# Optimization experiments

Measured on AMD Instinct MI355X. Metric: run time of the kernel, lower is better.

The kernel has to match this reference:

```python
import jax, jax.numpy as jnp
import numpy as np

N = 100000   # nodes
E = 3200000  # edges
G = 1024     # graphs in the batch
H = 64       # hidden_dim


def setup_inputs() -> dict:
    key = jax.random.key(0)
    ks = jax.random.split(key, 12)
    x = jax.random.normal(ks[0], (N, 1), dtype=jnp.float32)
    edge_index = jax.random.randint(ks[1], (2, E), 0, N, dtype=jnp.int32)
    batch = jnp.sort(jax.random.randint(ks[2], (N,), 0, G, dtype=jnp.int32))
    s = 0.1
    w1 = jax.random.normal(ks[3], (1, H), dtype=jnp.float32) * s
    b1 = jnp.zeros((H,), dtype=jnp.float32)
    w2 = jax.random.normal(ks[4], (H, H), dtype=jnp.float32) * s
    b2 = jnp.zeros((H,), dtype=jnp.float32)
    w3 = jax.random.normal(ks[5], (H, H), dtype=jnp.float32) * s
    b3 = jnp.zeros((H,), dtype=jnp.float32)
    fc_w = jax.random.normal(ks[6], (H, 1), dtype=jnp.float32) * s
    fc_b = jnp.zeros((1,), dtype=jnp.float32)
    return {"x": x, "edge_index": edge_index, "batch": batch,
            "w1": w1, "b1": b1, "w2": w2, "b2": b2, "w3": w3, "b3": b3,
            "fc_w": fc_w, "fc_b": fc_b}


def _gcn_norm(edge_index, n):
    # add self-loops: A_hat = A + I
    src = jnp.concatenate([edge_index[0], jnp.arange(n, dtype=edge_index.dtype)])
    dst = jnp.concatenate([edge_index[1], jnp.arange(n, dtype=edge_index.dtype)])
    deg = jax.ops.segment_sum(jnp.ones_like(dst, dtype=jnp.float32), dst, num_segments=n)
    dinv = jnp.where(deg > 0, jax.lax.rsqrt(deg), 0.0)
    norm = dinv[src] * dinv[dst]  # [E+N]
    return src, dst, norm


def _gcn_conv(x, w, b, src, dst, norm, n):
    h = x @ w                               # [N, H] transform first (PyG order)
    msg = h[src] * norm[:, None]            # gather + scale  [E+N, H]
    out = jax.ops.segment_sum(msg, dst, num_segments=n)  # scatter-add
    return out + b


def reference(x, edge_index, batch, w1, b1, w2, b2, w3, b3, fc_w, fc_b):
    n = x.shape[0]
    src, dst, norm = _gcn_norm(edge_index, n)
    h = jax.nn.relu(_gcn_conv(x, w1, b1, src, dst, norm, n))
    h = jax.nn.relu(_gcn_conv(h, w2, b2, src, dst, norm, n))
    h = jax.nn.relu(_gcn_conv(h, w3, b3, src, dst, norm, n))
    # global mean pool over graphs
    sums = jax.ops.segment_sum(h, batch, num_segments=G)                 # [G, H]
    cnts = jax.ops.segment_sum(jnp.ones((n,), jnp.float32), batch, num_segments=G)
    pooled = sums / jnp.maximum(cnts, 1.0)[:, None]
    return pooled @ fc_w + fc_b  # [G, 1]
```

## Files before the change

kernel.cpp:

```cpp
#include <hip/hip_runtime.h>
#include <hip/hip_bf16.h>


#define WS_ALIGN(x) (((x) + 255) & ~size_t(255))
#define NCHUNK 8
#define CSH 14
#define NB 32
#define RPW (NB / 4)
#define USH 17
#define UMASK 0x1FFFF
#define BKTMAX 256
#define SBS 512
#define SBKEYS (SBS * NCHUNK)
#define P1T 2048
#define PADGAP 1540

__device__ __forceinline__ float bf2f(unsigned short h) {
    union { unsigned u; float f; } t;
    t.u = ((unsigned)h) << 16;
    return t.f;
}
__device__ __forceinline__ unsigned short f2bf(float f) {
    union { float f; unsigned u; } t;
    t.f = f;
    unsigned r = t.u + 0x7FFF + ((t.u >> 16) & 1);
    return (unsigned short)(r >> 16);
}
__device__ __forceinline__ float bfLo(unsigned v) {
    union { unsigned u; float f; } t;
    t.u = v << 16;
    return t.f;
}
__device__ __forceinline__ float bfHi(unsigned v) {
    union { unsigned u; float f; } t;
    t.u = v & 0xFFFF0000u;
    return t.f;
}

__global__ __launch_bounds__(256) void k_zero(int g, int n, int* bucketCnt,
                                              int* gCursor, float* xs,
                                              unsigned short* bufA,
                                              unsigned short* bufB,
                                              float* gsum, float* gcnt) {
    int i = blockIdx.x * blockDim.x + threadIdx.x;
    if (i < BKTMAX) { bucketCnt[i] = 0; gCursor[i] = 0; }
    if (i < g) { gsum[i] = 0.f; gcnt[i] = 0.f; }
    if (i < 64) {
        bufA[(size_t)n * 64 + i] = 0;
        bufB[(size_t)n * 64 + i] = 0;
    }
    if (i == 0) xs[n] = 0.f;
}

__global__ __launch_bounds__(256) void k_cnt1(int e, const int* __restrict__ dst,
                                              int* __restrict__ bucketCnt) {
    __shared__ int c[BKTMAX];
    int tid = threadIdx.x;
    c[tid] = 0;
    __syncthreads();
    int base = blockIdx.x * P1T;
#pragma unroll
    for (int q = 0; q < P1T / 256; ++q) {
        int i = base + q * 256 + tid;
        if (i < e) atomicAdd(&c[dst[i] >> 9], 1);
    }
    __syncthreads();
    if (c[tid] > 0) atomicAdd(&bucketCnt[tid], c[tid]);
}

__global__ __launch_bounds__(256) void k_scanB(int nbkt, int e,
                                               const int* __restrict__ bucketCnt,
                                               int* __restrict__ bucketStart) {
    __shared__ int sd[256];
    int tid = threadIdx.x;
    int v = (tid < nbkt) ? bucketCnt[tid] : 0;
    sd[tid] = v;
    __syncthreads();
    for (int off = 1; off < 256; off <<= 1) {
        int t = (tid >= off) ? sd[tid - off] : 0;
        __syncthreads();
        sd[tid] += t;
        __syncthreads();
    }
    if (tid < nbkt) bucketStart[tid] = sd[tid] - v;
    if (tid == 0) bucketStart[nbkt] = e;
}

__global__ __launch_bounds__(256) void k_p1(int e, const int* __restrict__ src,
                                            const int* __restrict__ dst,
                                            const int* __restrict__ bucketStart,
                                            int* __restrict__ gCursor,
                                            int* __restrict__ pkbuf) {
    __shared__ int cnt[BKTMAX], exc[BKTMAX], cur[BKTMAX], bb[BKTMAX];
    __shared__ int sd[256];
    __shared__ int stage[P1T];
    __shared__ unsigned char stgb[P1T];
    int tid = threadIdx.x;
    cnt[tid] = 0;
    __syncthreads();
    int base = blockIdx.x * P1T;
    int m = e - base; if (m > P1T) m = P1T;
    int pk8[P1T / 256];
    int b8[P1T / 256];
#pragma unroll
    for (int q = 0; q < P1T / 256; ++q) {
        int li = q * 256 + tid;
        if (li < m) {
            int d = dst[base + li];
            int s = src[base + li];
            int b = d >> 9;
            b8[q] = b;
            pk8[q] = ((d & (SBS - 1)) << USH) | s;
            atomicAdd(&cnt[b], 1);
        }
    }
    __syncthreads();
    int cv = cnt[tid];
    sd[tid] = cv;
    __syncthreads();
    for (int off = 1; off < 256; off <<= 1) {
        int t = (tid >= off) ? sd[tid - off] : 0;
        __syncthreads();
        sd[tid] += t;
        __syncthreads();
    }
    exc[tid] = sd[tid] - cv;
    cur[tid] = sd[tid] - cv;
    if (cv > 0) bb[tid] = atomicAdd(&gCursor[tid], cv);
    __syncthreads();
#pragma unroll
    for (int q = 0; q < P1T / 256; ++q) {
        int li = q * 256 + tid;
        if (li < m) {
            int b = b8[q];
            int pos = atomicAdd(&cur[b], 1);
            stage[pos] = pk8[q];
            stgb[pos] = (unsigned char)b;
        }
    }
    __syncthreads();
#pragma unroll
    for (int q = 0; q < P1T / 256; ++q) {
        int p = q * 256 + tid;
        if (p < m) {
            int b = stgb[p];
            pkbuf[bucketStart[b] + bb[b] + (p - exc[b])] = stage[p];
        }
    }
}

__global__ __launch_bounds__(256) void k_p2(int n, const int* __restrict__ bucketStart,
                                            const int* __restrict__ pkbuf,
                                            const float* __restrict__ x,
                                            int* __restrict__ csr,
                                            int* __restrict__ bndRow,
                                            float* __restrict__ dinv,
                                            float* __restrict__ xs) {
    __shared__ int cnt[SBKEYS + 1];
    __shared__ int sd[256];
    __shared__ int padOff[SBS];
    __shared__ int padTotal_s;
    int sb = blockIdx.x, tid = threadIdx.x;
    int r0 = bucketStart[sb], r1 = bucketStart[sb + 1];
    int r0pad = r0 + sb * PADGAP;
    for (int k = tid; k < SBKEYS + 1; k += 256) cnt[k] = 0;
    __syncthreads();
    for (int i = r0 + tid; i < r1; i += 256) {
        int w = pkbuf[i];
        int key = ((w >> USH) << 3) | ((w & UMASK) >> CSH);
        atomicAdd(&cnt[key], 1);
    }
    __syncthreads();
    int base16 = tid * 16;
    int loc[16]; int s = 0;
#pragma unroll
    for (int j = 0; j < 16; ++j) { loc[j] = cnt[base16 + j]; s += loc[j]; }
    sd[tid] = s;
    __syncthreads();
    for (int off = 1; off < 256; off <<= 1) {
        int t = (tid >= off) ? sd[tid - off] : 0;
        __syncthreads();
        sd[tid] += t;
        __syncthreads();
    }
    int run = sd[tid] - s;
#pragma unroll
    for (int j = 0; j < 16; ++j) { cnt[base16 + j] = run; run += loc[j]; }
    if (tid == 255) cnt[SBKEYS] = run;
    __syncthreads();
    int d0 = tid * 2, d1 = tid * 2 + 1;
    int len0 = cnt[d0 * 8 + 8] - cnt[d0 * 8];
    int len1 = cnt[d1 * 8 + 8] - cnt[d1 * 8];
    int p0 = (-len0) & 3, p1 = (-len1) & 3;
    int tsum = p0 + p1;
    sd[tid] = tsum;
    __syncthreads();
    for (int off = 1; off < 256; off <<= 1) {
        int t = (tid >= off) ? sd[tid - off] : 0;
        __syncthreads();
        sd[tid] += t;
        __syncthreads();
    }
    int pexcl = sd[tid] - tsum;
    padOff[d0] = pexcl;
    padOff[d1] = pexcl + p0;
    if (tid == 255) padTotal_s = pexcl + tsum;
    __syncthreads();
    for (int dl = tid; dl < SBS; dl += 256) {
        int gbi = sb * 16 + (dl >> 5);
        int vi = dl & 31;
        int startp = r0pad + cnt[dl * 8] + padOff[dl];
        bndRow[gbi * 33 + vi] = startp;
        if (vi == 0 && dl > 0) bndRow[(gbi - 1) * 33 + 32] = startp;
        int v = sb * SBS + dl;
        if (v < n) {
            int len = cnt[dl * 8 + 8] - cnt[dl * 8];
            float di = 1.0f / sqrtf((float)(len + 1));
            dinv[v] = di;
            xs[v] = x[v] * di;
        }
        int padc = (-(cnt[dl * 8 + 8] - cnt[dl * 8])) & 3;
        int ps = r0pad + cnt[dl * 8 + 8] + padOff[dl];
        for (int j = 0; j < padc; ++j) csr[ps + j] = n;
    }
    if (tid == 0) {
        int endp = r0pad + cnt[SBKEYS] + padTotal_s;
        bndRow[(sb * 16 + 15) * 33 + 32] = endp;
        csr[endp] = n; csr[endp + 1] = n; csr[endp + 2] = n; csr[endp + 3] = n;
    }
    __syncthreads();
    for (int i = r0 + tid; i < r1; i += 256) {
        int w = pkbuf[i];
        int srcv = w & UMASK;
        int dl = w >> USH;
        int key = (dl << 3) | (srcv >> CSH);
        int pos = atomicAdd(&cnt[key], 1);
        csr[r0pad + pos + padOff[dl]] = srcv;
    }
}

__global__ __launch_bounds__(256, 8) void k_layer1(int n, const int* __restrict__ bndRow,
                                                   const int* __restrict__ csr,
                                                   const float* __restrict__ xs,
                                                   const float* __restrict__ dinv,
                                                   const float* __restrict__ w1,
                                                   const float* __restrict__ b1,
                                                   unsigned short* __restrict__ hs_out) {
    int tid = threadIdx.x;
    int r = tid >> 6, lane = tid & 63;
    float w1r = w1[lane], b1r = b1[lane];
    int wid = blockIdx.x * 4 + r;
    int stride = gridDim.x * 4;
    for (int v = wid; v < n; v += stride) {
        int bi = v >> 5, vi = v & 31;
        int s0 = bndRow[bi * 33 + vi], s1 = bndRow[bi * 33 + vi + 1];
        float acc = 0.f;
        for (int k = s0 + lane; k < s1; k += 64) acc += xs[csr[k]];
#pragma unroll
        for (int m = 32; m > 0; m >>= 1) acc += __shfl_xor(acc, m, 64);
        float dv = dinv[v];
        float s = (acc + xs[v]) * dv;
        hs_out[(size_t)v * 64 + lane] = f2bf(fmaxf(s * w1r + b1r, 0.f) * dv);
    }
}

#define GATHER_CORE                                                            \
    __shared__ float ws[64 * 64];                                              \
    __shared__ float rowl[4][64];                                              \
    __shared__ int bndL[NB + 1];                                               \
    int tid = threadIdx.x;                                                     \
    int lane = tid & 63;                                                       \
    int r = tid >> 6;                                                          \
    int h = lane >> 5;                                                         \
    int fi = lane & 31;                                                        \
    int v0 = blockIdx.x * NB;                                                  \
    const unsigned* hsu = (const unsigned*)hs_in;                              \
    for (int k = tid; k < 64 * 64; k += 256) ws[k] = w[k];                     \
    if (tid < NB + 1) bndL[tid] = bndRow[blockIdx.x * 33 + tid];               \
    float accLo[RPW], accHi[RPW];                                              \
    _Pragma("unroll")                                                          \
    for (int q = 0; q < RPW; ++q) {                                            \
        int v = v0 + q * 4 + r;                                                \
        unsigned sv = (v < n && h == 0) ? hsu[(size_t)v * 32 + fi] : 0u;       \
        accLo[q] = bfLo(sv);                                                   \
        accHi[q] = bfHi(sv);                                                   \
    }                                                                          \
    __syncthreads();                                                           \
    _Pragma("unroll")                                                          \
    for (int t = 0; t < RPW / 2; ++t) {                                        \
        int viA = (2 * t) * 4 + r;                                             \
        int viB = (2 * t + 1) * 4 + r;                                         \
        int ba = __builtin_amdgcn_readfirstlane(bndL[viA]);                    \
        int a1 = __builtin_amdgcn_readfirstlane(bndL[viA + 1]);                \
        int bb = __builtin_amdgcn_readfirstlane(bndL[viB]);                    \
        int b1_ = __builtin_amdgcn_readfirstlane(bndL[viB + 1]);               \
        int pa = (ba < a1) ? ba : bb;                                          \
        int pb = (bb < b1_) ? bb : ba;                                         \
        int uA0 = csr[pa], uA1 = csr[pa + 1], uA2 = csr[pa + 2], uA3 = csr[pa + 3]; \
        int uB0 = csr[pb], uB1 = csr[pb + 1], uB2 = csr[pb + 2], uB3 = csr[pb + 3]; \
        unsigned gA01 = hsu[(size_t)(h ? uA1 : uA0) * 32 + fi];                \
        unsigned gA23 = hsu[(size_t)(h ? uA3 : uA2) * 32 + fi];                \
        unsigned gB01 = hsu[(size_t)(h ? uB1 : uB0) * 32 + fi];                \
        unsigned gB23 = hsu[(size_t)(h ? uB3 : uB2) * 32 + fi];                \
        while (ba < a1 || bb < b1_) {                                          \
            int na = ba + 4, nb = bb + 4;                                      \
            int pa2 = (na < a1) ? na : ((nb < b1_) ? nb : pa);                 \
            int pb2 = (nb < b1_) ? nb : ((na < a1) ? na : pb);                 \
            int vA0 = csr[pa2], vA1 = csr[pa2 + 1], vA2 = csr[pa2 + 2], vA3 = csr[pa2 + 3]; \
            int vB0 = csr[pb2], vB1 = csr[pb2 + 1], vB2 = csr[pb2 + 2], vB3 = csr[pb2 + 3]; \
            unsigned nA01 = hsu[(size_t)(h ? vA1 : vA0) * 32 + fi];            \
            unsigned nA23 = hsu[(size_t)(h ? vA3 : vA2) * 32 + fi];            \
            unsigned nB01 = hsu[(size_t)(h ? vB1 : vB0) * 32 + fi];            \
            unsigned nB23 = hsu[(size_t)(h ? vB3 : vB2) * 32 + fi];            \
                            \
            float mA = (ba < a1) ? 1.f : 0.f;                                  \
            float mB = (bb < b1_) ? 1.f : 0.f;                                 \
            accLo[2 * t]     += (bfLo(gA01) + bfLo(gA23)) * mA;                \
            accHi[2 * t]     += (bfHi(gA01) + bfHi(gA23)) * mA;                \
            accLo[2 * t + 1] += (bfLo(gB01) + bfLo(gB23)) * mB;                \
            accHi[2 * t + 1] += (bfHi(gB01) + bfHi(gB23)) * mB;                \
            gA01 = nA01; gA23 = nA23; gB01 = nB01; gB23 = nB23;                \
            pa = pa2; pb = pb2;                                                \
            ba = na; bb = nb;                                                  \
        }                                                                      \
    }

__global__ __launch_bounds__(256, 4) void k_gg_mid(int n,
                                                   const int* __restrict__ bndRow,
                                                   const int* __restrict__ csr,
                                                   const unsigned short* __restrict__ hs_in,
                                                   const float* __restrict__ dinv,
                                                   const float* __restrict__ w,
                                                   const float* __restrict__ b,
                                                   unsigned short* __restrict__ hs_out) {
    GATHER_CORE
    float breg = b[lane];
#pragma unroll 1
    for (int q = 0; q < RPW; ++q) {
        int v = v0 + q * 4 + r;
        if (v >= n) continue;
        float dv = dinv[v];
        float lo = accLo[q]; lo += __shfl_xor(lo, 32, 64);
        float hi = accHi[q]; hi += __shfl_xor(hi, 32, 64);
        if (h == 0) {
            rowl[r][2 * fi] = lo * dv;
            rowl[r][2 * fi + 1] = hi * dv;
        }
        float o = breg;
#pragma unroll
        for (int k = 0; k < 64; ++k) o += rowl[r][k] * ws[k * 64 + lane];
        hs_out[(size_t)v * 64 + lane] = f2bf(fmaxf(o, 0.f) * dv);
    }
}

__global__ __launch_bounds__(256, 4) void k_gg_final(int n,
                                                     const int* __restrict__ bndRow,
                                                     const int* __restrict__ csr,
                                                     const unsigned short* __restrict__ hs_in,
                                                     const float* __restrict__ dinv,
                                                     const float* __restrict__ w,
                                                     const float* __restrict__ b,
                                                     const float* __restrict__ fcw,
                                                     float* __restrict__ dots) {
    GATHER_CORE
    float breg = b[lane];
    float freg = fcw[lane];
#pragma unroll 1
    for (int q = 0; q < RPW; ++q) {
        int v = v0 + q * 4 + r;
        if (v >= n) continue;
        float dv = dinv[v];
        float lo = accLo[q]; lo += __shfl_xor(lo, 32, 64);
        float hi = accHi[q]; hi += __shfl_xor(hi, 32, 64);
        if (h == 0) {
            rowl[r][2 * fi] = lo * dv;
            rowl[r][2 * fi + 1] = hi * dv;
        }
        float o = breg;
#pragma unroll
        for (int k = 0; k < 64; ++k) o += rowl[r][k] * ws[k * 64 + lane];
        float val = fmaxf(o, 0.f) * freg;
#pragma unroll
        for (int m = 32; m > 0; m >>= 1) val += __shfl_xor(val, m, 64);
        if (lane == 0) dots[v] = val;
    }
}

__global__ __launch_bounds__(256) void k_pool(int n, const float* __restrict__ dots,
                                              const int* __restrict__ batch,
                                              float* __restrict__ gsum,
                                              float* __restrict__ gcnt) {
    __shared__ float ls[64], lc[64];
    __shared__ int gmin_s;
    int tid = threadIdx.x;
    int i0 = blockIdx.x * 1024;
    if (tid == 0) gmin_s = batch[i0];
    if (tid < 64) { ls[tid] = 0.f; lc[tid] = 0.f; }
    __syncthreads();
    int gmin = gmin_s;
#pragma unroll
    for (int c = 0; c < 4; ++c) {
        int i = i0 + c * 256 + tid;
        if (i < n) {
            int g = batch[i];
            float d = dots[i];
            int rr = g - gmin;
            if (rr < 64) {
                atomicAdd(&ls[rr], d);
                atomicAdd(&lc[rr], 1.f);
            } else {
                atomicAdd(&gsum[g], d);
                atomicAdd(&gcnt[g], 1.f);
            }
        }
    }
    __syncthreads();
    if (tid < 64 && lc[tid] != 0.f) {
        atomicAdd(&gsum[gmin + tid], ls[tid]);
        atomicAdd(&gcnt[gmin + tid], lc[tid]);
    }
}

__global__ __launch_bounds__(256) void k_out(int g, const float* __restrict__ gsum,
                                             const float* __restrict__ gcnt,
                                             const float* __restrict__ fcb,
                                             float* __restrict__ out) {
    int i = blockIdx.x * blockDim.x + threadIdx.x;
    if (i < g) out[i] = gsum[i] / fmaxf(gcnt[i], 1.f) + fcb[0];
}

extern "C" void kernel_launch(void* const* d_in, const int* in_sizes, int n_in,
                              void* d_out, int out_size, void* d_ws, size_t ws_size,
                              hipStream_t stream) {
    const float* x    = (const float*)d_in[0];
    const int*   ei   = (const int*)d_in[1];
    const int*   batch= (const int*)d_in[2];
    const float* w1   = (const float*)d_in[3];
    const float* b1   = (const float*)d_in[4];
    const float* w2   = (const float*)d_in[5];
    const float* b2   = (const float*)d_in[6];
    const float* w3   = (const float*)d_in[7];
    const float* b3   = (const float*)d_in[8];
    const float* fcw  = (const float*)d_in[9];
    const float* fcb  = (const float*)d_in[10];
    float* out = (float*)d_out;

    const int N = in_sizes[0];
    const int E = in_sizes[1] / 2;
    const int G = out_size;
    const int H = 64;
    const int nbkt = (N + SBS - 1) / SBS;
    const int NBLK = (N + NB - 1) / NB;
    const int NBLKP = nbkt * 16;

    const int* src = ei;
    const int* dst = ei + E;

    char* p = (char*)d_ws;
    int*   bucketCnt   = (int*)p; p += WS_ALIGN(sizeof(int) * BKTMAX);
    int*   bucketStart = (int*)p; p += WS_ALIGN(sizeof(int) * (BKTMAX + 1));
    int*   gCursor     = (int*)p; p += WS_ALIGN(sizeof(int) * BKTMAX);
    int*   pkbuf       = (int*)p; p += WS_ALIGN(sizeof(int) * (size_t)E);
    int*   csr         = (int*)p; p += WS_ALIGN(sizeof(int) * ((size_t)E + (size_t)nbkt * PADGAP + 8));
    int*   bndRow      = (int*)p; p += WS_ALIGN(sizeof(int) * (size_t)NBLKP * 33);
    float* dinv        = (float*)p; p += WS_ALIGN(sizeof(float) * N);
    float* xs          = (float*)p; p += WS_ALIGN(sizeof(float) * (N + 1));
    unsigned short* bufA = (unsigned short*)p; p += WS_ALIGN(sizeof(unsigned short) * (size_t)(N + 1) * H);
    unsigned short* bufB = (unsigned short*)p; p += WS_ALIGN(sizeof(unsigned short) * (size_t)(N + 1) * H);
    float* dots        = (float*)p; p += WS_ALIGN(sizeof(float) * N);
    float* gsum        = (float*)p; p += WS_ALIGN(sizeof(float) * G);
    float* gcnt        = (float*)p; p += WS_ALIGN(sizeof(float) * G);

    const int B = 256;
    int gridZ    = ((G > BKTMAX ? G : BKTMAX) + B - 1) / B;
    int gridT    = (E + P1T - 1) / P1T;
    int gridG    = (G + B - 1) / B;
    int gridPool = (N + 1023) / 1024;
    int gridPers = 2048;
    if (gridPers * 4 > N) gridPers = (N + 3) / 4;

    k_zero<<<gridZ, B, 0, stream>>>(G, N, bucketCnt, gCursor, xs, bufA, bufB, gsum, gcnt);
    k_cnt1<<<gridT, B, 0, stream>>>(E, dst, bucketCnt);
    k_scanB<<<1, B, 0, stream>>>(nbkt, E, bucketCnt, bucketStart);
    k_p1<<<gridT, B, 0, stream>>>(E, src, dst, bucketStart, gCursor, pkbuf);
    k_p2<<<nbkt, B, 0, stream>>>(N, bucketStart, pkbuf, x, csr, bndRow, dinv, xs);
    k_layer1<<<gridPers, B, 0, stream>>>(N, bndRow, csr, xs, dinv, w1, b1, bufA);
    k_gg_mid<<<NBLK, B, 0, stream>>>(N, bndRow, csr, bufA, dinv, w2, b2, bufB);
    k_gg_final<<<NBLK, B, 0, stream>>>(N, bndRow, csr, bufB, dinv, w3, b3, fcw, dots);
    k_pool<<<gridPool, B, 0, stream>>>(N, dots, batch, gsum, gcnt);
    k_out<<<gridG, B, 0, stream>>>(G, gsum, gcnt, fcb, out);
}
```

Before: 327.2 us.

## Pre-scale CSR indices, pad rows to 8, and use single-row gather loop

Halves the super-bucket size (256 nodes, 512 buckets) so each thread owns one destination row in the CSR build. Rows are now padded to multiples of 8 instead of 4, and source indices are stored pre-shifted by 5 so the gather kernels index the bf16 feature array without a multiply. The gather core now processes one row at a time with an 8-edge software-pipelined loop and skips empty rows, replacing the paired-row loop with masking. The change trades more padding edges and less interleaving of independent rows for simpler addressing and wider per-iteration loads.

```diff
diff --git a/kernel.cpp b/kernel.cpp
--- a/kernel.cpp
+++ b/kernel.cpp
@@ -3,23 +3,17 @@
 
 
 #define WS_ALIGN(x) (((x) + 255) & ~size_t(255))
-#define NCHUNK 8
-#define CSH 14
 #define NB 32
 #define RPW (NB / 4)
 #define USH 17
-#define UMASK 0x1FFFF
-#define BKTMAX 256
-#define SBS 512
+#define BKTMAX 512
+#define SBS 256
+#define NCHUNK 8
+#define CSH 14
 #define SBKEYS (SBS * NCHUNK)
 #define P1T 2048
-#define PADGAP 1540
-
-__device__ __forceinline__ float bf2f(unsigned short h) {
-    union { unsigned u; float f; } t;
-    t.u = ((unsigned)h) << 16;
-    return t.f;
-}
+#define PADGAP 1792
+
 __device__ __forceinline__ unsigned short f2bf(float f) {
     union { float f; unsigned u; } t;
     t.f = f;
@@ -56,16 +50,17 @@
                                               int* __restrict__ bucketCnt) {
     __shared__ int c[BKTMAX];
     int tid = threadIdx.x;
-    c[tid] = 0;
+    c[tid] = 0; c[tid + 256] = 0;
     __syncthreads();
     int base = blockIdx.x * P1T;
 #pragma unroll
     for (int q = 0; q < P1T / 256; ++q) {
         int i = base + q * 256 + tid;
-        if (i < e) atomicAdd(&c[dst[i] >> 9], 1);
+        if (i < e) atomicAdd(&c[dst[i] >> 8], 1);
     }
     __syncthreads();
     if (c[tid] > 0) atomicAdd(&bucketCnt[tid], c[tid]);
+    if (c[tid + 256] > 0) atomicAdd(&bucketCnt[tid + 256], c[tid + 256]);
 }
 
 __global__ __launch_bounds__(256) void k_scanB(int nbkt, int e,
@@ -73,8 +68,11 @@
                                                int* __restrict__ bucketStart) {
     __shared__ int sd[256];
     int tid = threadIdx.x;
-    int v = (tid < nbkt) ? bucketCnt[tid] : 0;
-    sd[tid] = v;
+    int i0 = tid * 2;
+    int v0 = (i0 < nbkt) ? bucketCnt[i0] : 0;
+    int v1 = (i0 + 1 < nbkt) ? bucketCnt[i0 + 1] : 0;
+    int ts = v0 + v1;
+    sd[tid] = ts;
     __syncthreads();
     for (int off = 1; off < 256; off <<= 1) {
         int t = (tid >= off) ? sd[tid - off] : 0;
@@ -82,7 +80,9 @@
         sd[tid] += t;
         __syncthreads();
     }
-    if (tid < nbkt) bucketStart[tid] = sd[tid] - v;
+    int excl = sd[tid] - ts;
+    if (i0 < nbkt) bucketStart[i0] = excl;
+    if (i0 + 1 < nbkt) bucketStart[i0 + 1] = excl + v0;
     if (tid == 0) bucketStart[nbkt] = e;
 }
 
@@ -94,9 +94,9 @@
     __shared__ int cnt[BKTMAX], exc[BKTMAX], cur[BKTMAX], bb[BKTMAX];
     __shared__ int sd[256];
     __shared__ int stage[P1T];
-    __shared__ unsigned char stgb[P1T];
+    __shared__ unsigned short stgb[P1T];
     int tid = threadIdx.x;
-    cnt[tid] = 0;
+    cnt[tid] = 0; cnt[tid + 256] = 0;
     __syncthreads();
     int base = blockIdx.x * P1T;
     int m = e - base; if (m > P1T) m = P1T;
@@ -108,15 +108,17 @@
         if (li < m) {
             int d = dst[base + li];
             int s = src[base + li];
-            int b = d >> 9;
+            int b = d >> 8;
             b8[q] = b;
             pk8[q] = ((d & (SBS - 1)) << USH) | s;
             atomicAdd(&cnt[b], 1);
         }
     }
     __syncthreads();
-    int cv = cnt[tid];
-    sd[tid] = cv;
+    int i0 = tid * 2;
+    int c0 = cnt[i0], c1 = cnt[i0 + 1];
+    int ts = c0 + c1;
+    sd[tid] = ts;
     __syncthreads();
     for (int off = 1; off < 256; off <<= 1) {
         int t = (tid >= off) ? sd[tid - off] : 0;
@@ -124,9 +126,11 @@
         sd[tid] += t;
         __syncthreads();
     }
-    exc[tid] = sd[tid] - cv;
-    cur[tid] = sd[tid] - cv;
-    if (cv > 0) bb[tid] = atomicAdd(&gCursor[tid], cv);
+    int ex = sd[tid] - ts;
+    exc[i0] = ex;       exc[i0 + 1] = ex + c0;
+    cur[i0] = ex;       cur[i0 + 1] = ex + c0;
+    if (c0 > 0) bb[i0] = atomicAdd(&gCursor[i0], c0);
+    if (c1 > 0) bb[i0 + 1] = atomicAdd(&gCursor[i0 + 1], c1);
     __syncthreads();
 #pragma unroll
     for (int q = 0; q < P1T / 256; ++q) {
@@ -135,7 +139,7 @@
             int b = b8[q];
             int pos = atomicAdd(&cur[b], 1);
             stage[pos] = pk8[q];
-            stgb[pos] = (unsigned char)b;
+            stgb[pos] = (unsigned short)b;
         }
     }
     __syncthreads();
@@ -167,14 +171,14 @@
     __syncthreads();
     for (int i = r0 + tid; i < r1; i += 256) {
         int w = pkbuf[i];
-        int key = ((w >> USH) << 3) | ((w & UMASK) >> CSH);
+        int key = ((w >> USH) << 3) | ((w & ((1 << USH) - 1)) >> CSH);
         atomicAdd(&cnt[key], 1);
     }
     __syncthreads();
-    int base16 = tid * 16;
-    int loc[16]; int s = 0;
-#pragma unroll
-    for (int j = 0; j < 16; ++j) { loc[j] = cnt[base16 + j]; s += loc[j]; }
+    int base8 = tid * 8;
+    int loc[8]; int s = 0;
+#pragma unroll
+    for (int j = 0; j < 8; ++j) { loc[j] = cnt[base8 + j]; s += loc[j]; }
     sd[tid] = s;
     __syncthreads();
     for (int off = 1; off < 256; off <<= 1) {
@@ -185,15 +189,12 @@
     }
     int run = sd[tid] - s;
 #pragma unroll
-    for (int j = 0; j < 16; ++j) { cnt[base16 + j] = run; run += loc[j]; }
+    for (int j = 0; j < 8; ++j) { cnt[base8 + j] = run; run += loc[j]; }
     if (tid == 255) cnt[SBKEYS] = run;
     __syncthreads();
-    int d0 = tid * 2, d1 = tid * 2 + 1;
-    int len0 = cnt[d0 * 8 + 8] - cnt[d0 * 8];
-    int len1 = cnt[d1 * 8 + 8] - cnt[d1 * 8];
-    int p0 = (-len0) & 3, p1 = (-len1) & 3;
-    int tsum = p0 + p1;
-    sd[tid] = tsum;
+    int lenR = cnt[tid * 8 + 8] - cnt[tid * 8];
+    int padR = (-lenR) & 7;
+    sd[tid] = padR;
     __syncthreads();
     for (int off = 1; off < 256; off <<= 1) {
         int t = (tid >= off) ? sd[tid - off] : 0;
@@ -201,41 +202,38 @@
         sd[tid] += t;
         __syncthreads();
     }
-    int pexcl = sd[tid] - tsum;
-    padOff[d0] = pexcl;
-    padOff[d1] = pexcl + p0;
-    if (tid == 255) padTotal_s = pexcl + tsum;
-    __syncthreads();
-    for (int dl = tid; dl < SBS; dl += 256) {
-        int gbi = sb * 16 + (dl >> 5);
+    int pexcl = sd[tid] - padR;
+    padOff[tid] = pexcl;
+    if (tid == 255) padTotal_s = pexcl + padR;
+    __syncthreads();
+    {
+        int dl = tid;
+        int gbi = sb * 8 + (dl >> 5);
         int vi = dl & 31;
         int startp = r0pad + cnt[dl * 8] + padOff[dl];
         bndRow[gbi * 33 + vi] = startp;
         if (vi == 0 && dl > 0) bndRow[(gbi - 1) * 33 + 32] = startp;
         int v = sb * SBS + dl;
         if (v < n) {
-            int len = cnt[dl * 8 + 8] - cnt[dl * 8];
-            float di = 1.0f / sqrtf((float)(len + 1));
+            float di = 1.0f / sqrtf((float)(lenR + 1));
             dinv[v] = di;
             xs[v] = x[v] * di;
         }
-        int padc = (-(cnt[dl * 8 + 8] - cnt[dl * 8])) & 3;
         int ps = r0pad + cnt[dl * 8 + 8] + padOff[dl];
-        for (int j = 0; j < padc; ++j) csr[ps + j] = n;
+        for (int j = 0; j < padR; ++j) csr[ps + j] = n << 5;
     }
     if (tid == 0) {
         int endp = r0pad + cnt[SBKEYS] + padTotal_s;
-        bndRow[(sb * 16 + 15) * 33 + 32] = endp;
-        csr[endp] = n; csr[endp + 1] = n; csr[endp + 2] = n; csr[endp + 3] = n;
+        bndRow[(sb * 8 + 7) * 33 + 32] = endp;
     }
     __syncthreads();
     for (int i = r0 + tid; i < r1; i += 256) {
         int w = pkbuf[i];
-        int srcv = w & UMASK;
+        int srcv = w & ((1 << USH) - 1);
         int dl = w >> USH;
         int key = (dl << 3) | (srcv >> CSH);
         int pos = atomicAdd(&cnt[key], 1);
-        csr[r0pad + pos + padOff[dl]] = srcv;
+        csr[r0pad + pos + padOff[dl]] = srcv << 5;
     }
 }
 
@@ -255,7 +253,7 @@
         int bi = v >> 5, vi = v & 31;
         int s0 = bndRow[bi * 33 + vi], s1 = bndRow[bi * 33 + vi + 1];
         float acc = 0.f;
-        for (int k = s0 + lane; k < s1; k += 64) acc += xs[csr[k]];
+        for (int k = s0 + lane; k < s1; k += 64) acc += xs[csr[k] >> 5];
 #pragma unroll
         for (int m = 32; m > 0; m >>= 1) acc += __shfl_xor(acc, m, 64);
         float dv = dinv[v];
@@ -287,41 +285,36 @@
     }                                                                          \
     __syncthreads();                                                           \
     _Pragma("unroll")                                                          \
-    for (int t = 0; t < RPW / 2; ++t) {                                        \
-        int viA = (2 * t) * 4 + r;                                             \
-        int viB = (2 * t + 1) * 4 + r;                                         \
-        int ba = __builtin_amdgcn_readfirstlane(bndL[viA]);                    \
-        int a1 = __builtin_amdgcn_readfirstlane(bndL[viA + 1]);                \
-        int bb = __builtin_amdgcn_readfirstlane(bndL[viB]);                    \
-        int b1_ = __builtin_amdgcn_readfirstlane(bndL[viB + 1]);               \
-        int pa = (ba < a1) ? ba : bb;                                          \
-        int pb = (bb < b1_) ? bb : ba;                                         \
-        int uA0 = csr[pa], uA1 = csr[pa + 1], uA2 = csr[pa + 2], uA3 = csr[pa + 3]; \
-        int uB0 = csr[pb], uB1 = csr[pb + 1], uB2 = csr[pb + 2], uB3 = csr[pb + 3]; \
-        unsigned gA01 = hsu[(size_t)(h ? uA1 : uA0) * 32 + fi];                \
-        unsigned gA23 = hsu[(size_t)(h ? uA3 : uA2) * 32 + fi];                \
-        unsigned gB01 = hsu[(size_t)(h ? uB1 : uB0) * 32 + fi];                \
-        unsigned gB23 = hsu[(size_t)(h ? uB3 : uB2) * 32 + fi];                \
-        while (ba < a1 || bb < b1_) {                                          \
-            int na = ba + 4, nb = bb + 4;                                      \
-            int pa2 = (na < a1) ? na : ((nb < b1_) ? nb : pa);                 \
-            int pb2 = (nb < b1_) ? nb : ((na < a1) ? na : pb);                 \
-            int vA0 = csr[pa2], vA1 = csr[pa2 + 1], vA2 = csr[pa2 + 2], vA3 = csr[pa2 + 3]; \
-            int vB0 = csr[pb2], vB1 = csr[pb2 + 1], vB2 = csr[pb2 + 2], vB3 = csr[pb2 + 3]; \
-            unsigned nA01 = hsu[(size_t)(h ? vA1 : vA0) * 32 + fi];            \
-            unsigned nA23 = hsu[(size_t)(h ? vA3 : vA2) * 32 + fi];            \
-            unsigned nB01 = hsu[(size_t)(h ? vB1 : vB0) * 32 + fi];            \
-            unsigned nB23 = hsu[(size_t)(h ? vB3 : vB2) * 32 + fi];            \
-                            \
-            float mA = (ba < a1) ? 1.f : 0.f;                                  \
-            float mB = (bb < b1_) ? 1.f : 0.f;                                 \
-            accLo[2 * t]     += (bfLo(gA01) + bfLo(gA23)) * mA;                \
-            accHi[2 * t]     += (bfHi(gA01) + bfHi(gA23)) * mA;                \
-            accLo[2 * t + 1] += (bfLo(gB01) + bfLo(gB23)) * mB;                \
-            accHi[2 * t + 1] += (bfHi(gB01) + bfHi(gB23)) * mB;                \
-            gA01 = nA01; gA23 = nA23; gB01 = nB01; gB23 = nB23;                \
-            pa = pa2; pb = pb2;                                                \
-            ba = na; bb = nb;                                                  \
+    for (int q = 0; q < RPW; ++q) {                                            \
+        int vi = q * 4 + r;                                                    \
+        int p  = __builtin_amdgcn_readfirstlane(bndL[vi]);                     \
+        int s1 = __builtin_amdgcn_readfirstlane(bndL[vi + 1]);                 \
+        if (p < s1) {                                                          \
+            int c0 = csr[p],     c1 = csr[p + 1];                              \
+            int c2 = csr[p + 2], c3 = csr[p + 3];                              \
+            int c4 = csr[p + 4], c5 = csr[p + 5];                              \
+            int c6 = csr[p + 6], c7 = csr[p + 7];                              \
+            unsigned g0 = hsu[(h ? c1 : c0) + fi];                             \
+            unsigned g1 = hsu[(h ? c3 : c2) + fi];                             \
+            unsigned g2 = hsu[(h ? c5 : c4) + fi];                             \
+            unsigned g3 = hsu[(h ? c7 : c6) + fi];                             \
+            p += 8;                                                            \
+            while (p < s1) {                                                   \
+                int d0 = csr[p],     d1 = csr[p + 1];                          \
+                int d2 = csr[p + 2], d3 = csr[p + 3];                          \
+                int d4 = csr[p + 4], d5 = csr[p + 5];                          \
+                int d6 = csr[p + 6], d7 = csr[p + 7];                          \
+                unsigned n0 = hsu[(h ? d1 : d0) + fi];                         \
+                unsigned n1 = hsu[(h ? d3 : d2) + fi];                         \
+                unsigned n2 = hsu[(h ? d5 : d4) + fi];                         \
+                unsigned n3 = hsu[(h ? d7 : d6) + fi];                         \
+                accLo[q] += (bfLo(g0) + bfLo(g1)) + (bfLo(g2) + bfLo(g3));     \
+                accHi[q] += (bfHi(g0) + bfHi(g1)) + (bfHi(g2) + bfHi(g3));     \
+                g0 = n0; g1 = n1; g2 = n2; g3 = n3;                            \
+                p += 8;                                                        \
+            }                                                                  \
+            accLo[q] += (bfLo(g0) + bfLo(g1)) + (bfLo(g2) + bfLo(g3));         \
+            accHi[q] += (bfHi(g0) + bfHi(g1)) + (bfHi(g2) + bfHi(g3));         \
         }                                                                      \
     }
 
@@ -451,7 +444,7 @@
     const int H = 64;
     const int nbkt = (N + SBS - 1) / SBS;
     const int NBLK = (N + NB - 1) / NB;
-    const int NBLKP = nbkt * 16;
+    const int NBLKP = nbkt * 8;
 
     const int* src = ei;
     const int* dst = ei + E;
@@ -461,7 +454,7 @@
     int*   bucketStart = (int*)p; p += WS_ALIGN(sizeof(int) * (BKTMAX + 1));
     int*   gCursor     = (int*)p; p += WS_ALIGN(sizeof(int) * BKTMAX);
     int*   pkbuf       = (int*)p; p += WS_ALIGN(sizeof(int) * (size_t)E);
-    int*   csr         = (int*)p; p += WS_ALIGN(sizeof(int) * ((size_t)E + (size_t)nbkt * PADGAP + 8));
+    int*   csr         = (int*)p; p += WS_ALIGN(sizeof(int) * ((size_t)E + (size_t)nbkt * PADGAP + 16));
     int*   bndRow      = (int*)p; p += WS_ALIGN(sizeof(int) * (size_t)NBLKP * 33);
     float* dinv        = (float*)p; p += WS_ALIGN(sizeof(float) * N);
     float* xs          = (float*)p; p += WS_ALIGN(sizeof(float) * (N + 1));
@@ -472,7 +465,8 @@
     float* gcnt        = (float*)p; p += WS_ALIGN(sizeof(float) * G);
 
     const int B = 256;
-    int gridZ    = ((G > BKTMAX ? G : BKTMAX) + B - 1) / B;
+    int gmax     = (G > BKTMAX ? G : BKTMAX);
+    int gridZ    = (gmax + B - 1) / B;
     int gridT    = (E + P1T - 1) / P1T;
     int gridG    = (G + B - 1) / B;
     int gridPool = (N + 1023) / 1024;
```

After: 344.7 us. 1.05x slower.
